# Performance work log

Measured on AMD Instinct MI355X. Metric: run time of the kernel, lower is better.

The kernel has to match this reference:

```python
import jax, jax.numpy as jnp
import numpy as np


def _ramp_filter(H):
    # skimage-style Fourier ramp filter: 2*|f| with f = fftfreq(H)
    f = np.fft.fftfreq(H)
    return (2.0 * np.abs(f)).astype(np.float32)


def setup_inputs() -> dict:
    key = jax.random.key(0)
    N, H_in, W_in, D_out = 8, 768, 360, 512
    radon_image = jax.random.normal(key, (N, 1, H_in, W_in), dtype=jnp.float32)
    hG = jnp.asarray(_ramp_filter(H_in)).reshape(1, 1, H_in, 1)
    return {"radon_image": radon_image, "hG": hG, "D_out": D_out}


def reference(radon_image, hG, D_out):
    N, _, H, W = radon_image.shape
    D = D_out
    # --- Fourier-domain ramp filtering (2D FFT, multiply by real filter along detector axis, real ifft) ---
    X = jnp.fft.fft2(radon_image[:, 0])                     # [N, H, W] complex
    h = hG[0, 0, :, 0]                                      # [H]
    filt = jnp.real(jnp.fft.ifft2(X * h[None, :, None])).astype(radon_image.dtype)  # [N, H, W]

    # --- backprojection grids (matches np.mgrid / tG construction) ---
    Xg, Yg = jnp.meshgrid(jnp.arange(D), jnp.arange(D), indexing="ij")
    xpr = (Xg - D // 2).astype(jnp.float32)
    ypr = (Yg - D // 2).astype(jnp.float32)
    th = (jnp.pi / 180.0) * jnp.linspace(0.0, 180.0, W, endpoint=False)  # [W]
    txs = -1.0 + jnp.arange(W, dtype=jnp.float32) * (2.0 / (W - 1))     # [W]

    hH = H // 2
    sy = (H - 1) / 2.0   # align_corners=True y scale
    sx = (W - 1) / 2.0   # align_corners=True x scale

    def body(recon, angle):
        th_i, tx_i = angle
        t = ypr * jnp.cos(th_i) - xpr * jnp.sin(th_i)       # [D, D]
        py = (t / hH + 1.0) * sy                            # pixel y coords [D, D]
        px = (tx_i + 1.0) * sx                              # scalar pixel x coord
        x0 = jnp.floor(px).astype(jnp.int32)
        wx = px - x0
        y0 = jnp.floor(py).astype(jnp.int32)
        wy = py - y0

        def samp_col(xi):
            vx = ((xi >= 0) & (xi < W)).astype(filt.dtype)
            col = filt[:, :, jnp.clip(xi, 0, W - 1)]        # [N, H]

            def samp_y(yi):
                vy = ((yi >= 0) & (yi < H)).astype(filt.dtype)
                return col[:, jnp.clip(yi, 0, H - 1)] * vy  # [N, D, D] zero-padded

            v = samp_y(y0) * (1.0 - wy) + samp_y(y0 + 1) * wy
            return v * vx

        val = samp_col(x0) * (1.0 - wx) + samp_col(x0 + 1) * wx  # [N, D, D]
        return recon + val, None

    recon0 = jnp.zeros((N, D, D), dtype=radon_image.dtype)
    recon, _ = jax.lax.scan(body, recon0, (th, txs))
    return (recon * (jnp.pi / (2.0 * W)))[:, None]          # [N, 1, D, D]
```

## Files before the change

### kernel.cpp

```cpp
#include <hip/hip_runtime.h>
#include <math.h>

#define N_IMG 8
#define H 768
#define W 360
#define D 512
#define SY 383.5f
#define SX 179.5f
#define SC 0.00436332312998582394f

typedef __fp16 h2 __attribute__((ext_vector_type(2)));
struct H2X2 { h2 a, b; };
typedef short short8 __attribute__((ext_vector_type(8)));
typedef float f32x4 __attribute__((ext_vector_type(4)));

__device__ inline unsigned bf16pair(float a, float b) {
    unsigned ua = __builtin_bit_cast(unsigned, a);
    unsigned ub = __builtin_bit_cast(unsigned, b);
    ua += 0x7FFFu + ((ua >> 16) & 1u);
    ub += 0x7FFFu + ((ub >> 16) & 1u);
    return (ua >> 16) | (ub & 0xFFFF0000u);
}

__global__ void build_g_kernel(const float* __restrict__ hG, float* __restrict__ g) {
    int m = blockIdx.x;
    int lane = threadIdx.x;
    float s = 0.f;
#pragma unroll
    for (int q = 0; q < 12; ++q) {
        int k = lane + 64 * q;
        int prod = (k * m) % H;
        float angr = (float)prod * 0.00818123086872313911f;
        s += hG[k] * cosf(angr);
    }
#pragma unroll
    for (int off = 32; off > 0; off >>= 1) s += __shfl_down(s, off);
    if (lane == 0) g[m] = s * (1.0f / (float)H);
}

__global__ void build_ang_kernel(float2* __restrict__ ang) {
    int i = blockIdx.x * 64 + threadIdx.x;
    if (i < W) {
        float th = (float)i * 0.00872664625997164788f;
        float r = SY / 384.0f;
        ang[i] = make_float2(cosf(th) * r, -sinf(th) * r);
    }
}

#define KSTEPS 10

__global__ void build_bg_kernel(const float* __restrict__ g, uint4* __restrict__ Bg) {
    int idx = blockIdx.x * 64 + threadIdx.x;
    int L  = idx & 63;
    int tj = idx >> 6;
    int nn = (tj & 3) * 16 + (L & 15);
    int kb = (tj >> 2) * 32 + (L >> 4) * 8;
    float bf[8];
#pragma unroll
    for (int s = 0; s < 8; ++s) {
        int d = nn + 128 - (kb + s);
        d += (d < 0) ? H : 0;
        bf[s] = g[d];
    }
    uint4 pk = {bf16pair(bf[0], bf[1]), bf16pair(bf[2], bf[3]),
                bf16pair(bf[4], bf[5]), bf16pair(bf[6], bf[7])};
    Bg[idx] = pk;
}

__global__ __launch_bounds__(256)
void filt_gemm_kernel(const float* __restrict__ radon, const uint4* __restrict__ Bg,
                      float* __restrict__ colc) {
    __shared__ __align__(16) unsigned short As[2][64 * 40];

    const int n  = blockIdx.z;
    const int i0 = blockIdx.y * 64;
    const int y0 = blockIdx.x * 64;
    const int tid = threadIdx.x;
    const int wv  = tid >> 6;
    const int L   = tid & 63;

    const int mbase = (y0 + H - 128) % H;

    const int iS = tid >> 2;
    const int oS = tid & 3;

    float w0 = 0.f, w1 = 0.f;
    int x0 = 0, x1 = 0;
    {
        int ig = i0 + iS;
        if (ig < W) {
            float tx = -1.0f + (float)ig * (2.0f / (float)(W - 1));
            float px = (tx + 1.0f) * SX;
            float fx = floorf(px);
            float wx = px - fx;
            int xi = (int)fx;
            if (xi >= 0 && xi < W)         { x0 = xi;     w0 = 1.0f - wx; }
            if (xi + 1 >= 0 && xi + 1 < W) { x1 = xi + 1; w1 = wx; }
        }
    }
    const float* rn = radon + (size_t)n * H * W;

    f32x4 acc[4];
#pragma unroll
    for (int j = 0; j < 4; ++j) acc[j] = (f32x4){0.f, 0.f, 0.f, 0.f};

    {
        float af[8];
        int mb = mbase + oS * 8;
#pragma unroll
        for (int s = 0; s < 8; ++s) {
            int m = mb + s;
            m -= (m >= H) ? H : 0;
            af[s] = w0 * rn[m * W + x0] + w1 * rn[m * W + x1];
        }
        uint4 pk = {bf16pair(af[0], af[1]), bf16pair(af[2], af[3]),
                    bf16pair(af[4], af[5]), bf16pair(af[6], af[7])};
        *(uint4*)&As[0][iS * 40 + oS * 8] = pk;
    }
    __syncthreads();

    for (int t = 0; t < KSTEPS; ++t) {
        float af[8];
        if (t + 1 < KSTEPS) {
            int mb = mbase + 32 * (t + 1) + oS * 8;
#pragma unroll
            for (int s = 0; s < 8; ++s) {
                int m = mb + s;
                m -= (m >= H) ? H : 0;
                af[s] = w0 * rn[m * W + x0] + w1 * rn[m * W + x1];
            }
        }

        const int cb = t & 1;
        short8 a = __builtin_bit_cast(short8,
                       *(const uint4*)&As[cb][(wv * 16 + (L & 15)) * 40 + (L >> 4) * 8]);
#pragma unroll
        for (int j = 0; j < 4; ++j) {
            short8 b = __builtin_bit_cast(short8, Bg[(t * 4 + j) * 64 + L]);
            acc[j] = __builtin_amdgcn_mfma_f32_16x16x32_bf16(a, b, acc[j], 0, 0, 0);
        }

        if (t + 1 < KSTEPS) {
            uint4 pk = {bf16pair(af[0], af[1]), bf16pair(af[2], af[3]),
                        bf16pair(af[4], af[5]), bf16pair(af[6], af[7])};
            *(uint4*)&As[cb ^ 1][iS * 40 + oS * 8] = pk;
        }
        __syncthreads();
    }

#pragma unroll
    for (int j = 0; j < 4; ++j) {
#pragma unroll
        for (int r = 0; r < 4; ++r) {
            int ig = i0 + wv * 16 + (L >> 4) * 4 + r;
            if (ig < W) {
                int y = y0 + j * 16 + (L & 15);
                colc[((size_t)n * W + ig) * H + y] = acc[j][r] * SC;
            }
        }
    }
}

__global__ __launch_bounds__(512, 8)
void backproj_kernel(const float* __restrict__ colc, const float2* __restrict__ angv,
                     float* __restrict__ outb) {
    __shared__ __align__(16) H2X2 colh[2][H];

    const int bid = blockIdx.x;
    const int bz  = bid & 7;
    const int tle = bid >> 3;
    const int g4 = (bz >> 2) * 4;
    const int aq = bz & 3;
    const int a0 = aq * (W / 4);
    const int u0 = (tle >> 3) * 32;
    const int v0 = (tle & 7) * 64;
    const int tid = threadIdx.x;
    const int lane = tid & 63;
    const int tu = tid >> 6;

    const float vf = (float)(v0 + lane - D / 2);
    float uf[4];
#pragma unroll
    for (int r = 0; r < 4; ++r) uf[r] = (float)(u0 + tu + 8 * r - D / 2);

    const h2 hz = {(__fp16)0.f, (__fp16)0.f};
    float acc[4][4];
    h2 haccA[4], haccB[4];
#pragma unroll
    for (int r = 0; r < 4; ++r) {
#pragma unroll
        for (int nn = 0; nn < 4; ++nn) acc[r][nn] = 0.f;
        haccA[r] = hz;
        haccB[r] = hz;
    }

    const float* c0p = colc + (size_t)(g4 + 0) * W * H;
    const float* c1p = colc + (size_t)(g4 + 1) * W * H;
    const float* c2p = colc + (size_t)(g4 + 2) * W * H;
    const float* c3p = colc + (size_t)(g4 + 3) * W * H;

    const int y1 = tid;
    const int y2 = tid + 512;

    {
        const int ab = a0 * H;
        float d0 = c0p[ab + y1], d1 = c1p[ab + y1], d2 = c2p[ab + y1], d3 = c3p[ab + y1];
        colh[0][y1] = (H2X2){__builtin_amdgcn_cvt_pkrtz(d0, d1),
                             __builtin_amdgcn_cvt_pkrtz(d2, d3)};
        if (tid < 256) {
            float e0 = c0p[ab + y2], e1 = c1p[ab + y2], e2 = c2p[ab + y2], e3 = c3p[ab + y2];
            colh[0][y2] = (H2X2){__builtin_amdgcn_cvt_pkrtz(e0, e1),
                                 __builtin_amdgcn_cvt_pkrtz(e2, e3)};
        }
    }
    __syncthreads();

    for (int j = 0; j < W / 4; ++j) {
        int a = a0 + j;
        int an = (j + 1 < W / 4) ? (a + 1) : a;
        const int ab = an * H;
        float d0 = c0p[ab + y1], d1 = c1p[ab + y1], d2 = c2p[ab + y1], d3 = c3p[ab + y1];
        float e0 = 0.f, e1 = 0.f, e2 = 0.f, e3 = 0.f;
        if (tid < 256) { e0 = c0p[ab + y2]; e1 = c1p[ab + y2]; e2 = c2p[ab + y2]; e3 = c3p[ab + y2]; }

        const int cb2 = j & 1;
        float2 AB = angv[a];
        float base = fmaf(vf, AB.x, SY);
#pragma unroll
        for (int r = 0; r < 4; ++r) {
            float py = fmaf(uf[r], AB.y, base);
            float wy = __builtin_amdgcn_fractf(py);
            int iy = (int)py;
            uint2 lo_raw = *(const uint2*)&colh[cb2][iy];
            uint2 hi_raw = *(const uint2*)&colh[cb2][iy + 1];
            H2X2 lo = __builtin_bit_cast(H2X2, lo_raw);
            H2X2 hi = __builtin_bit_cast(H2X2, hi_raw);
            h2 wy2 = __builtin_amdgcn_cvt_pkrtz(wy, wy);
            haccA[r] += lo.a + wy2 * (hi.a - lo.a);
            haccB[r] += lo.b + wy2 * (hi.b - lo.b);
        }

        if ((j & 15) == 15) {
#pragma unroll
            for (int r = 0; r < 4; ++r) {
                acc[r][0] += (float)haccA[r].x;
                acc[r][1] += (float)haccA[r].y;
                acc[r][2] += (float)haccB[r].x;
                acc[r][3] += (float)haccB[r].y;
                haccA[r] = hz;
                haccB[r] = hz;
            }
        }

        {
            colh[cb2 ^ 1][y1] = (H2X2){__builtin_amdgcn_cvt_pkrtz(d0, d1),
                                       __builtin_amdgcn_cvt_pkrtz(d2, d3)};
            if (tid < 256)
                colh[cb2 ^ 1][y2] = (H2X2){__builtin_amdgcn_cvt_pkrtz(e0, e1),
                                           __builtin_amdgcn_cvt_pkrtz(e2, e3)};
        }
        __syncthreads();
    }

#pragma unroll
    for (int r = 0; r < 4; ++r) {
        acc[r][0] += (float)haccA[r].x;
        acc[r][1] += (float)haccA[r].y;
        acc[r][2] += (float)haccB[r].x;
        acc[r][3] += (float)haccB[r].y;
        int u = u0 + tu + 8 * r;
#pragma unroll
        for (int nn = 0; nn < 4; ++nn) {
            size_t idx = ((size_t)(g4 + nn) * D + u) * D + v0 + lane;
            atomicAdd(&outb[idx], acc[r][nn]);
        }
    }
}

__global__ void zero_kernel(float4* __restrict__ o) {
    int i = blockIdx.x * 512 + threadIdx.x;
    o[i] = make_float4(0.f, 0.f, 0.f, 0.f);
}

extern "C" void kernel_launch(void* const* d_in, const int* in_sizes, int n_in,
                              void* d_out, int out_size, void* d_ws, size_t ws_size,
                              hipStream_t stream) {
    const float* radon = (const float*)d_in[0];
    const float* hG    = (const float*)d_in[1];
    float* out = (float*)d_out;

    float*  g    = (float*)d_ws;
    float2* ang  = (float2*)((char*)d_ws + 4096);
    float*  colc = (float*)((char*)d_ws + 16384);
    uint4*  Bg   = (uint4*)((char*)d_ws + 8864768);

    zero_kernel<<<1024, 512, 0, stream>>>((float4*)out);
    build_g_kernel<<<H, 64, 0, stream>>>(hG, g);
    build_ang_kernel<<<(W + 63) / 64, 64, 0, stream>>>(ang);
    build_bg_kernel<<<40, 64, 0, stream>>>(g, Bg);
    filt_gemm_kernel<<<dim3(H / 64, 384 / 64, N_IMG), 256, 0, stream>>>(radon, Bg, colc);
    backproj_kernel<<<1024, 512, 0, stream>>>(colc, ang, out);
}
```

Baseline: 199.8 us.

## Prepack bf16 A operand in separate kernel and store fp16 interleaved columns

A new kernel computes the x-interpolated radon rows once, tiles them through LDS, and stores them as bf16 in MFMA-ready layout. The GEMM then reads A fragments straight from global memory with no LDS double buffer or barriers. The GEMM output is now written as fp16 with four images interleaved, so the backprojection loads one 8-byte word per row instead of four floats and no longer converts. This cuts redundant strided radon gathers and halves the intermediate traffic, at the cost of an extra launch, strided 2-byte scattered stores, and fp16 rounding one stage earlier.

```diff
diff --git a/kernel.cpp b/kernel.cpp
--- a/kernel.cpp
+++ b/kernel.cpp
@@ -8,6 +8,8 @@
 #define SY 383.5f
 #define SX 179.5f
 #define SC 0.00436332312998582394f
+#define NC 24
+#define IPAD 384
 
 typedef __fp16 h2 __attribute__((ext_vector_type(2)));
 struct H2X2 { h2 a, b; };
@@ -68,86 +70,87 @@
 }
 
 __global__ __launch_bounds__(256)
-void filt_gemm_kernel(const float* __restrict__ radon, const uint4* __restrict__ Bg,
-                      float* __restrict__ colc) {
-    __shared__ __align__(16) unsigned short As[2][64 * 40];
-
+void build_rc_kernel(const float* __restrict__ radon, uint4* __restrict__ rcC) {
+    __shared__ float xs[32][69];
+
+    const int i0 = blockIdx.x * 64;
+    const int c  = blockIdx.y;
+    const int n  = blockIdx.z;
+    const int tid = threadIdx.x;
+    const int xw0 = (i0 > 0) ? i0 - 1 : 0;
+    const float* rn = radon + (size_t)n * H * W;
+
+    {
+        int mrow = tid >> 3;
+        int xoff = tid & 7;
+        const float* src = rn + (size_t)(32 * c + mrow) * W;
+#pragma unroll
+        for (int s = 0; s < 9; ++s) {
+            int xo = xoff + 8 * s;
+            int x = xw0 + xo;
+            if (xo < 66 && x < W) xs[mrow][xo] = src[x];
+        }
+    }
+    __syncthreads();
+
+    const int il  = tid >> 2;
+    const int oct = tid & 3;
+    const int i = i0 + il;
+
+    float w0 = 0.f, w1 = 0.f;
+    int lx0 = 0, lx1 = 0;
+    if (i < W) {
+        float tx = -1.0f + (float)i * (2.0f / (float)(W - 1));
+        float px = (tx + 1.0f) * SX;
+        float fx = floorf(px);
+        float wx = px - fx;
+        int xi = (int)fx;
+        if (xi >= 0 && xi < W)         { w0 = 1.0f - wx; lx0 = xi - xw0; }
+        if (xi + 1 >= 0 && xi + 1 < W) { w1 = wx;        lx1 = xi + 1 - xw0; }
+    }
+
+    float v[8];
+#pragma unroll
+    for (int s = 0; s < 8; ++s) {
+        int ml = oct * 8 + s;
+        v[s] = w0 * xs[ml][lx0] + w1 * xs[ml][lx1];
+    }
+    uint4 pk = {bf16pair(v[0], v[1]), bf16pair(v[2], v[3]),
+                bf16pair(v[4], v[5]), bf16pair(v[6], v[7])};
+    rcC[(((size_t)n * NC + c) * IPAD + i) * 4 + oct] = pk;
+}
+
+__global__ __launch_bounds__(256)
+void filt_gemm_kernel(const uint4* __restrict__ rcC, const uint4* __restrict__ Bg,
+                      unsigned short* __restrict__ colp) {
     const int n  = blockIdx.z;
     const int i0 = blockIdx.y * 64;
     const int y0 = blockIdx.x * 64;
-    const int tid = threadIdx.x;
-    const int wv  = tid >> 6;
-    const int L   = tid & 63;
-
-    const int mbase = (y0 + H - 128) % H;
-
-    const int iS = tid >> 2;
-    const int oS = tid & 3;
-
-    float w0 = 0.f, w1 = 0.f;
-    int x0 = 0, x1 = 0;
-    {
-        int ig = i0 + iS;
-        if (ig < W) {
-            float tx = -1.0f + (float)ig * (2.0f / (float)(W - 1));
-            float px = (tx + 1.0f) * SX;
-            float fx = floorf(px);
-            float wx = px - fx;
-            int xi = (int)fx;
-            if (xi >= 0 && xi < W)         { x0 = xi;     w0 = 1.0f - wx; }
-            if (xi + 1 >= 0 && xi + 1 < W) { x1 = xi + 1; w1 = wx; }
-        }
-    }
-    const float* rn = radon + (size_t)n * H * W;
+    const int wv = threadIdx.x >> 6;
+    const int L  = threadIdx.x & 63;
+
+    const int c0 = (y0 / 32 + 20) % NC;
+    const uint4* An = rcC + (size_t)n * NC * IPAD * 4;
+    const int arow = i0 + wv * 16 + (L & 15);
+    const int aoff = L >> 4;
 
     f32x4 acc[4];
 #pragma unroll
     for (int j = 0; j < 4; ++j) acc[j] = (f32x4){0.f, 0.f, 0.f, 0.f};
 
-    {
-        float af[8];
-        int mb = mbase + oS * 8;
-#pragma unroll
-        for (int s = 0; s < 8; ++s) {
-            int m = mb + s;
-            m -= (m >= H) ? H : 0;
-            af[s] = w0 * rn[m * W + x0] + w1 * rn[m * W + x1];
-        }
-        uint4 pk = {bf16pair(af[0], af[1]), bf16pair(af[2], af[3]),
-                    bf16pair(af[4], af[5]), bf16pair(af[6], af[7])};
-        *(uint4*)&As[0][iS * 40 + oS * 8] = pk;
-    }
-    __syncthreads();
-
     for (int t = 0; t < KSTEPS; ++t) {
-        float af[8];
-        if (t + 1 < KSTEPS) {
-            int mb = mbase + 32 * (t + 1) + oS * 8;
-#pragma unroll
-            for (int s = 0; s < 8; ++s) {
-                int m = mb + s;
-                m -= (m >= H) ? H : 0;
-                af[s] = w0 * rn[m * W + x0] + w1 * rn[m * W + x1];
-            }
-        }
-
-        const int cb = t & 1;
-        short8 a = __builtin_bit_cast(short8,
-                       *(const uint4*)&As[cb][(wv * 16 + (L & 15)) * 40 + (L >> 4) * 8]);
+        int c = c0 + t;
+        c -= (c >= NC) ? NC : 0;
+        short8 a = __builtin_bit_cast(short8, An[((size_t)c * IPAD + arow) * 4 + aoff]);
 #pragma unroll
         for (int j = 0; j < 4; ++j) {
             short8 b = __builtin_bit_cast(short8, Bg[(t * 4 + j) * 64 + L]);
             acc[j] = __builtin_amdgcn_mfma_f32_16x16x32_bf16(a, b, acc[j], 0, 0, 0);
         }
-
-        if (t + 1 < KSTEPS) {
-            uint4 pk = {bf16pair(af[0], af[1]), bf16pair(af[2], af[3]),
-                        bf16pair(af[4], af[5]), bf16pair(af[6], af[7])};
-            *(uint4*)&As[cb ^ 1][iS * 40 + oS * 8] = pk;
-        }
-        __syncthreads();
-    }
-
+    }
+
+    const int g = n >> 2, slot = n & 3;
+    unsigned short* cp = colp + (size_t)g * W * H * 4 + slot;
 #pragma unroll
     for (int j = 0; j < 4; ++j) {
 #pragma unroll
@@ -155,21 +158,22 @@
             int ig = i0 + wv * 16 + (L >> 4) * 4 + r;
             if (ig < W) {
                 int y = y0 + j * 16 + (L & 15);
-                colc[((size_t)n * W + ig) * H + y] = acc[j][r] * SC;
+                _Float16 hv = (_Float16)(acc[j][r] * SC);
+                cp[((size_t)ig * H + y) * 4] = __builtin_bit_cast(unsigned short, hv);
             }
         }
     }
 }
 
 __global__ __launch_bounds__(512, 8)
-void backproj_kernel(const float* __restrict__ colc, const float2* __restrict__ angv,
-                     float* __restrict__ outb) {
+void backproj_kernel(const unsigned short* __restrict__ colp,
+                     const float2* __restrict__ angv, float* __restrict__ outb) {
     __shared__ __align__(16) H2X2 colh[2][H];
 
     const int bid = blockIdx.x;
     const int bz  = bid & 7;
     const int tle = bid >> 3;
-    const int g4 = (bz >> 2) * 4;
+    const int g  = bz >> 2;
     const int aq = bz & 3;
     const int a0 = aq * (W / 4);
     const int u0 = (tle >> 3) * 32;
@@ -194,23 +198,18 @@
         haccB[r] = hz;
     }
 
-    const float* c0p = colc + (size_t)(g4 + 0) * W * H;
-    const float* c1p = colc + (size_t)(g4 + 1) * W * H;
-    const float* c2p = colc + (size_t)(g4 + 2) * W * H;
-    const float* c3p = colc + (size_t)(g4 + 3) * W * H;
+    const uint2* cp = (const uint2*)colp + (size_t)g * W * H;
 
     const int y1 = tid;
     const int y2 = tid + 512;
 
     {
         const int ab = a0 * H;
-        float d0 = c0p[ab + y1], d1 = c1p[ab + y1], d2 = c2p[ab + y1], d3 = c3p[ab + y1];
-        colh[0][y1] = (H2X2){__builtin_amdgcn_cvt_pkrtz(d0, d1),
-                             __builtin_amdgcn_cvt_pkrtz(d2, d3)};
+        uint2 d = cp[ab + y1];
+        colh[0][y1] = __builtin_bit_cast(H2X2, d);
         if (tid < 256) {
-            float e0 = c0p[ab + y2], e1 = c1p[ab + y2], e2 = c2p[ab + y2], e3 = c3p[ab + y2];
-            colh[0][y2] = (H2X2){__builtin_amdgcn_cvt_pkrtz(e0, e1),
-                                 __builtin_amdgcn_cvt_pkrtz(e2, e3)};
+            uint2 e = cp[ab + y2];
+            colh[0][y2] = __builtin_bit_cast(H2X2, e);
         }
     }
     __syncthreads();
@@ -219,9 +218,9 @@
         int a = a0 + j;
         int an = (j + 1 < W / 4) ? (a + 1) : a;
         const int ab = an * H;
-        float d0 = c0p[ab + y1], d1 = c1p[ab + y1], d2 = c2p[ab + y1], d3 = c3p[ab + y1];
-        float e0 = 0.f, e1 = 0.f, e2 = 0.f, e3 = 0.f;
-        if (tid < 256) { e0 = c0p[ab + y2]; e1 = c1p[ab + y2]; e2 = c2p[ab + y2]; e3 = c3p[ab + y2]; }
+        uint2 d = cp[ab + y1];
+        uint2 e = make_uint2(0u, 0u);
+        if (tid < 256) e = cp[ab + y2];
 
         const int cb2 = j & 1;
         float2 AB = angv[a];
@@ -252,13 +251,8 @@
             }
         }
 
-        {
-            colh[cb2 ^ 1][y1] = (H2X2){__builtin_amdgcn_cvt_pkrtz(d0, d1),
-                                       __builtin_amdgcn_cvt_pkrtz(d2, d3)};
-            if (tid < 256)
-                colh[cb2 ^ 1][y2] = (H2X2){__builtin_amdgcn_cvt_pkrtz(e0, e1),
-                                           __builtin_amdgcn_cvt_pkrtz(e2, e3)};
-        }
+        colh[cb2 ^ 1][y1] = __builtin_bit_cast(H2X2, d);
+        if (tid < 256) colh[cb2 ^ 1][y2] = __builtin_bit_cast(H2X2, e);
         __syncthreads();
     }
 
@@ -271,7 +265,7 @@
         int u = u0 + tu + 8 * r;
 #pragma unroll
         for (int nn = 0; nn < 4; ++nn) {
-            size_t idx = ((size_t)(g4 + nn) * D + u) * D + v0 + lane;
+            size_t idx = ((size_t)(g * 4 + nn) * D + u) * D + v0 + lane;
             atomicAdd(&outb[idx], acc[r][nn]);
         }
     }
@@ -291,13 +285,15 @@
 
     float*  g    = (float*)d_ws;
     float2* ang  = (float2*)((char*)d_ws + 4096);
-    float*  colc = (float*)((char*)d_ws + 16384);
-    uint4*  Bg   = (uint4*)((char*)d_ws + 8864768);
+    uint4*  Bg   = (uint4*)((char*)d_ws + 8192);
+    unsigned short* colp = (unsigned short*)((char*)d_ws + 65536);
+    uint4*  rcC  = (uint4*)((char*)d_ws + 4489216);
 
     zero_kernel<<<1024, 512, 0, stream>>>((float4*)out);
     build_g_kernel<<<H, 64, 0, stream>>>(hG, g);
     build_ang_kernel<<<(W + 63) / 64, 64, 0, stream>>>(ang);
     build_bg_kernel<<<40, 64, 0, stream>>>(g, Bg);
-    filt_gemm_kernel<<<dim3(H / 64, 384 / 64, N_IMG), 256, 0, stream>>>(radon, Bg, colc);
-    backproj_kernel<<<1024, 512, 0, stream>>>(colc, ang, out);
-}
+    build_rc_kernel<<<dim3(6, NC, N_IMG), 256, 0, stream>>>(radon, rcC);
+    filt_gemm_kernel<<<dim3(H / 64, 384 / 64, N_IMG), 256, 0, stream>>>(rcC, Bg, colp);
+    backproj_kernel<<<1024, 512, 0, stream>>>(colp, ang, out);
+}
```

Result: faster. 172.8 us (-13.5%).
